# Kernel tuning notes

Hardware: AMD Instinct MI355X
Metric: run time of the kernel (lower is better)

## Reference

```python
import jax, jax.numpy as jnp
import numpy as np

HEADS = 16
HD = 64
LN_EPS = 1e-5


def swish(x):
    return x * jax.nn.sigmoid(x)


def layer_norm(x):
    mu = jnp.mean(x, axis=-1, keepdims=True)
    var = jnp.var(x, axis=-1, keepdims=True)
    return (x - mu) * jax.lax.rsqrt(var + LN_EPS)


def setup_inputs() -> dict:
    key = jax.random.key(0)
    ks = jax.random.split(key, 5)
    B, L, D = 4, 2048, 1024
    x = jax.random.normal(ks[0], (B, L, D), dtype=jnp.float32)
    W_fc = jax.random.normal(ks[1], (D, HEADS * HD * 3), dtype=jnp.float32) * (1.0 / np.sqrt(D))
    b_fc = jax.random.normal(ks[2], (HEADS * HD * 3,), dtype=jnp.float32) * 0.01
    W_fc2 = jax.random.normal(ks[3], (HEADS * HD, D), dtype=jnp.float32) * (1.0 / np.sqrt(HEADS * HD))
    b_fc2 = jax.random.normal(ks[4], (D,), dtype=jnp.float32) * 0.01
    return {"x": x, "W_fc": W_fc, "b_fc": b_fc, "W_fc2": W_fc2, "b_fc2": b_fc2}


def reference(x, W_fc, b_fc, W_fc2, b_fc2):
    B, L, D = x.shape
    # fused QKV projection with swish activation (dropout is identity in eval)
    qkv = swish(jnp.einsum('bld,de->ble', x, W_fc) + b_fc)
    qkv = qkv.reshape(B, L, HEADS, 3 * HD)
    q, k, v = jnp.split(qkv, 3, axis=-1)  # each [B, L, H, hd]
    # NOTE: original scales by sqrt(length), not sqrt(hd)
    scores = jnp.einsum('bwhd,bmhd->bhwm', q, k) / jnp.sqrt(jnp.float32(L))
    att = jax.nn.softmax(scores, axis=-1)  # [B, H, L, L]
    new_v = jnp.einsum('bhwm,bmhd->bwhd', att, v).reshape(B, L, HEADS * HD)
    m = swish(jnp.einsum('ble,ed->bld', new_v, W_fc2) + b_fc2)
    return layer_norm(x + m)
```

## Files before the change

kernel.cpp:

```cpp
#include <hip/hip_runtime.h>
#include <cstddef>
#include <cstdint>

typedef unsigned short u16;
typedef __attribute__((ext_vector_type(8))) short short8;
typedef __attribute__((ext_vector_type(4))) float floatx4;

#define C1_SCALE 0.031882111f
#define LOG2E    1.4426950408889634f

__device__ __forceinline__ u16 f2bf(float f) {
    union { float f; unsigned int i; } v; v.f = f;
    unsigned int b = v.i;
    b += 0x7FFFu + ((b >> 16) & 1u);
    return (u16)(b >> 16);
}

__device__ __forceinline__ unsigned pk2bf(float lo, float hi) {
#if __has_builtin(__builtin_amdgcn_cvt_pk_bf16_f32)
    auto v = __builtin_amdgcn_cvt_pk_bf16_f32(lo, hi);
    union { decltype(v) b; unsigned u; } c; c.b = v; return c.u;
#else
    return (unsigned)f2bf(lo) | ((unsigned)f2bf(hi) << 16);
#endif
}
__device__ __forceinline__ int4 pack8bf(float4 a, float4 b) {
    union { unsigned u[4]; int4 v; } c;
    c.u[0] = pk2bf(a.x, a.y); c.u[1] = pk2bf(a.z, a.w);
    c.u[2] = pk2bf(b.x, b.y); c.u[3] = pk2bf(b.z, b.w);
    return c.v;
}
__device__ __forceinline__ float fastrcp(float x) {
#if __has_builtin(__builtin_amdgcn_rcpf)
    return __builtin_amdgcn_rcpf(x);
#else
    return 1.0f / x;
#endif
}
__device__ __forceinline__ float swishf(float s) {
    float e = __builtin_amdgcn_exp2f(-s * LOG2E);
    return s * fastrcp(1.0f + e);
}
__device__ __forceinline__ void glds16(const void* g, void* l) {
    __builtin_amdgcn_global_load_lds(
        (const __attribute__((address_space(1))) void*)g,
        (__attribute__((address_space(3))) void*)l, 16, 0, 0);
}

__global__ __launch_bounds__(256) void prep_kernel(
    const float* __restrict__ x,     u16* __restrict__ xb,
    const float* __restrict__ W_fc,  u16* __restrict__ WfcT,
    const float* __restrict__ W_fc2, u16* __restrict__ Wfc2T)
{
    const int id = blockIdx.x;
    if (id < 4096) {
        const size_t i = ((size_t)id * 256 + threadIdx.x) * 8;
        float4 a = *(const float4*)&x[i];
        float4 b = *(const float4*)&x[i + 4];
        *(int4*)&xb[i] = pack8bf(a, b);
        return;
    }
    __shared__ u16 t[32][33];
    const float* src; u16* dst; int R, C, bx, by;
    if (id < 7168) {
        const int w = id - 4096;
        bx = w % 96; by = w / 96; src = W_fc; dst = WfcT; R = 1024; C = 3072;
    } else {
        const int w = id - 7168;
        bx = w % 32; by = w / 32; src = W_fc2; dst = Wfc2T; R = 1024; C = 1024;
    }
    const int tx = threadIdx.x & 31, ty = threadIdx.x >> 5;
    const int r0 = by * 32, c0 = bx * 32;
#pragma unroll
    for (int i = 0; i < 4; ++i)
        t[ty + i * 8][tx] = f2bf(src[(size_t)(r0 + ty + i * 8) * C + c0 + tx]);
    __syncthreads();
#pragma unroll
    for (int i = 0; i < 4; ++i)
        dst[(size_t)(c0 + ty + i * 8) * R + r0 + tx] = t[tx][ty + i * 8];
}

#define GEMM_STAGE(AP, BP, Kdim)                                              \
    {                                                                          \
        _Pragma("unroll")                                                      \
        for (int i = 0; i < 4; ++i) {                                          \
            const int row = i * 32 + (tid >> 3);                               \
            const int gp  = (tid & 7) ^ (row & 7);                             \
            glds16(&AP[(size_t)(row0 + row) * Kdim + k0 + gp * 8],             \
                   &As[i * 32 + wid * 8][0]);                                  \
            glds16(&BP[(size_t)(col0 + row) * Kdim + k0 + gp * 8],             \
                   &Bs[i * 32 + wid * 8][0]);                                  \
        }                                                                      \
    }

#define GEMM_COMPUTE()                                                         \
    {                                                                          \
        _Pragma("unroll")                                                      \
        for (int kc = 0; kc < 2; ++kc) {                                       \
            short8 af[4], bf[4];                                               \
            const int gl = ((kc * 4 + quad) ^ (l16 & 7)) * 8;                  \
            _Pragma("unroll")                                                  \
            for (int mt = 0; mt < 4; ++mt)                                     \
                af[mt] = *(const short8*)&As[wm * 64 + mt * 16 + l16][gl];     \
            _Pragma("unroll")                                                  \
            for (int nt = 0; nt < 4; ++nt)                                     \
                bf[nt] = *(const short8*)&Bs[wn * 64 + nt * 16 + l16][gl];     \
            _Pragma("unroll")                                                  \
            for (int mt = 0; mt < 4; ++mt)                                     \
                _Pragma("unroll")                                              \
                for (int nt = 0; nt < 4; ++nt)                                 \
                    acc[mt][nt] = __builtin_amdgcn_mfma_f32_16x16x32_bf16(     \
                        af[mt], bf[nt], acc[mt][nt], 0, 0, 0);                 \
        }                                                                      \
    }

__global__ __launch_bounds__(256) void gemm_qkv_kernel(
    const u16* __restrict__ A, const u16* __restrict__ BT,
    const float* __restrict__ bias, u16* __restrict__ qk, u16* __restrict__ vT)
{
    const int K = 1024;
    const int tid  = threadIdx.x;
    const int wid  = tid >> 6;
    const int lane = tid & 63;
    const int quad = lane >> 4;
    const int l16  = lane & 15;
    const int wm = wid >> 1, wn = wid & 1;
    const int row0 = blockIdx.y * 128, col0 = blockIdx.x * 128;

    __shared__ __align__(16) u16 As[128][64];
    __shared__ __align__(16) u16 Bs[128][64];

    floatx4 acc[4][4] = {};

    for (int k0 = 0; k0 < K; k0 += 64) {
        if (k0) __syncthreads();
        GEMM_STAGE(A, BT, K);
        __syncthreads();
        GEMM_COMPUTE();
    }

    float bb[4];
#pragma unroll
    for (int nt = 0; nt < 4; ++nt)
        bb[nt] = bias[col0 + wn * 64 + nt * 16 + l16];

    const int b = row0 >> 11;
#pragma unroll
    for (int mt = 0; mt < 4; ++mt) {
        const int rbase = row0 + wm * 64 + mt * 16 + quad * 4;
        const int l0 = rbase & 2047;
#pragma unroll
        for (int nt = 0; nt < 4; ++nt) {
            const int c = col0 + wn * 64 + nt * 16 + l16;
            const unsigned h = (unsigned)c / 192u;
            const int w = c - (int)h * 192;
            float sw[4];
#pragma unroll
            for (int r = 0; r < 4; ++r)
                sw[r] = swishf(acc[mt][nt][r] + bb[nt]);
            if (w < 128) {
                const float scl = (w >= 64) ? C1_SCALE : 1.0f;
#pragma unroll
                for (int r = 0; r < 4; ++r)
                    qk[(size_t)(rbase + r) * 2048 + h * 128 + w] = f2bf(sw[r] * scl);
            } else {
                union { unsigned u[2]; uint2 v; } pk;
                pk.u[0] = pk2bf(sw[0], sw[1]);
                pk.u[1] = pk2bf(sw[2], sw[3]);
                *(uint2*)&vT[(size_t)((b * 16 + (int)h) * 64 + (w - 128)) * 2048 + l0] = pk.v;
            }
        }
    }
}

__global__ __launch_bounds__(256) void gemm_out_kernel(
    const u16* __restrict__ A, const u16* __restrict__ BT,
    const float* __restrict__ bias, const float* __restrict__ xres,
    float* __restrict__ out)
{
    const int K = 1024, N = 1024;
    const int tid  = threadIdx.x;
    const int wid  = tid >> 6;
    const int lane = tid & 63;
    const int quad = lane >> 4;
    const int l16  = lane & 15;
    const int wm = wid >> 1, wn = wid & 1;
    const int row0 = blockIdx.y * 128, col0 = blockIdx.x * 128;

    __shared__ __align__(16) u16 As[128][64];
    __shared__ __align__(16) u16 Bs[128][64];

    floatx4 acc[4][4] = {};

    for (int k0 = 0; k0 < K; k0 += 64) {
        if (k0) __syncthreads();
        GEMM_STAGE(A, BT, K);
        __syncthreads();
        GEMM_COMPUTE();
    }

    float bb[4];
#pragma unroll
    for (int nt = 0; nt < 4; ++nt)
        bb[nt] = bias[col0 + wn * 64 + nt * 16 + l16];

#pragma unroll
    for (int mt = 0; mt < 4; ++mt) {
#pragma unroll
        for (int nt = 0; nt < 4; ++nt) {
#pragma unroll
            for (int r = 0; r < 4; ++r) {
                int row = row0 + wm * 64 + mt * 16 + quad * 4 + r;
                int col = col0 + wn * 64 + nt * 16 + l16;
                float sw = swishf(acc[mt][nt][r] + bb[nt]);
                out[(size_t)row * N + col] = xres[(size_t)row * N + col] + sw;
            }
        }
    }
}

__global__ __launch_bounds__(256) void attn_kernel(
    const u16* __restrict__ qk, const u16* __restrict__ vT,
    u16* __restrict__ newv)
{
    const int tid  = threadIdx.x;
    const int wid  = tid >> 6;
    const int lane = tid & 63;
    const int quad = lane >> 4;
    const int l16  = lane & 15;
    const int id = blockIdx.x;
    const int qt = id >> 6;
    const int hb = id & 63;
    const int h  = hb & 15;
    const int b  = hb >> 4;

    const u16* qkb = qk + (size_t)b * 2048 * 2048;
    const u16* vTb = vT + (size_t)(b * 16 + h) * 64 * 2048;

    short8 qf[2][2];
#pragma unroll
    for (int it = 0; it < 2; ++it) {
        const int qrow = qt * 128 + (wid * 2 + it) * 16 + l16;
        const u16* qp = &qkb[(size_t)qrow * 2048 + h * 128];
        qf[it][0] = *(const short8*)&qp[quad * 8];
        qf[it][1] = *(const short8*)&qp[32 + quad * 8];
    }

    const short one = (short)0x3F80;
    const short8 ones = {one, one, one, one, one, one, one, one};

    __shared__ __align__(16) u16 Ks[128][64];
    __shared__ __align__(16) u16 Vt[64][128];
    __shared__ __align__(16) u16 Ps[4][16][64];

    const int krow_l = tid >> 3;
    const int kgp    = (tid & 7) ^ (krow_l & 7);
    const int vrow_l = tid >> 4;
    const int vg     = tid & 15;
    const int vgp    = ((vg >> 3) << 3) | ((vg & 7) ^ (vrow_l & 7));

    floatx4 oacc[2][4] = {};
    floatx4 sumacc[2] = {};

    for (int kt = 0; kt < 16; ++kt) {
        const int k0 = kt * 128;
        if (kt) __syncthreads();
#pragma unroll
        for (int c = 0; c < 4; ++c)
            glds16(&qkb[(size_t)(k0 + c * 32 + krow_l) * 2048 + h * 128 + 64 + kgp * 8],
                   &Ks[c * 32 + wid * 8][0]);
#pragma unroll
        for (int c = 0; c < 4; ++c)
            glds16(&vTb[(size_t)(c * 16 + vrow_l) * 2048 + k0 + vgp * 8],
                   &Vt[c * 16 + wid * 4][0]);
        __syncthreads();

#pragma unroll
        for (int s = 0; s < 2; ++s) {
            floatx4 sacc[2][4] = {};
#pragma unroll
            for (int kc = 0; kc < 2; ++kc) {
                const int gl = ((kc * 4 + quad) ^ (l16 & 7)) * 8;
#pragma unroll
                for (int nt = 0; nt < 4; ++nt) {
                    short8 kf = *(const short8*)&Ks[s * 64 + nt * 16 + l16][gl];
                    sacc[0][nt] = __builtin_amdgcn_mfma_f32_16x16x32_bf16(kf, qf[0][kc], sacc[0][nt], 0, 0, 0);
                    sacc[1][nt] = __builtin_amdgcn_mfma_f32_16x16x32_bf16(kf, qf[1][kc], sacc[1][nt], 0, 0, 0);
                }
            }

#pragma unroll
            for (int it = 0; it < 2; ++it) {
#pragma unroll
                for (int nt = 0; nt < 4; ++nt) {
                    float p0 = __builtin_amdgcn_exp2f(sacc[it][nt][0]);
                    float p1 = __builtin_amdgcn_exp2f(sacc[it][nt][1]);
                    float p2 = __builtin_amdgcn_exp2f(sacc[it][nt][2]);
                    float p3 = __builtin_amdgcn_exp2f(sacc[it][nt][3]);
                    union { unsigned u[2]; uint2 v; } pk;
                    pk.u[0] = pk2bf(p0, p1);
                    pk.u[1] = pk2bf(p2, p3);
                    const int col = (((nt * 2 + (quad >> 1)) ^ (l16 & 7)) * 8) + (quad & 1) * 4;
                    *(uint2*)&Ps[wid][l16][col] = pk.v;
                }
#pragma unroll
                for (int kc = 0; kc < 2; ++kc) {
                    const int gl = ((kc * 4 + quad) ^ (l16 & 7)) * 8;
                    short8 pf = *(const short8*)&Ps[wid][l16][gl];
                    sumacc[it] = __builtin_amdgcn_mfma_f32_16x16x32_bf16(ones, pf, sumacc[it], 0, 0, 0);
#pragma unroll
                    for (int nt = 0; nt < 4; ++nt) {
                        short8 vf = *(const short8*)&Vt[nt * 16 + l16][s * 64 + gl];
                        oacc[it][nt] = __builtin_amdgcn_mfma_f32_16x16x32_bf16(vf, pf, oacc[it][nt], 0, 0, 0);
                    }
                }
            }
        }
    }

#pragma unroll
    for (int it = 0; it < 2; ++it) {
        const float inv = fastrcp(sumacc[it][0]);
        const int row = qt * 128 + (wid * 2 + it) * 16 + l16;
        u16* orow = &newv[((size_t)b * 2048 + row) * 1024 + h * 64];
#pragma unroll
        for (int nt = 0; nt < 4; ++nt) {
            union { unsigned u[2]; uint2 v; } pk;
            pk.u[0] = pk2bf(oacc[it][nt][0] * inv, oacc[it][nt][1] * inv);
            pk.u[1] = pk2bf(oacc[it][nt][2] * inv, oacc[it][nt][3] * inv);
            *(uint2*)&orow[nt * 16 + quad * 4] = pk.v;
        }
    }
}

__global__ __launch_bounds__(256) void ln_kernel(
    const float* __restrict__ y, float* __restrict__ out)
{
    const int row = blockIdx.x;
    const int tid = threadIdx.x;
    const float* yr = y + (size_t)row * 1024;
    float v[4];
    float s1 = 0.f, s2 = 0.f;
#pragma unroll
    for (int i = 0; i < 4; ++i) {
        v[i] = yr[tid + i * 256];
        s1 += v[i];
        s2 += v[i] * v[i];
    }
#pragma unroll
    for (int off = 1; off < 64; off <<= 1) {
        s1 += __shfl_xor(s1, off, 64);
        s2 += __shfl_xor(s2, off, 64);
    }
    __shared__ float red1[4], red2[4];
    const int wid = tid >> 6, lane = tid & 63;
    if (lane == 0) { red1[wid] = s1; red2[wid] = s2; }
    __syncthreads();
    s1 = red1[0] + red1[1] + red1[2] + red1[3];
    s2 = red2[0] + red2[1] + red2[2] + red2[3];
    const float mu   = s1 * (1.0f / 1024.0f);
    const float var  = s2 * (1.0f / 1024.0f) - mu * mu;
    const float rstd = rsqrtf(var + 1e-5f);
    float* orow = out + (size_t)row * 1024;
#pragma unroll
    for (int i = 0; i < 4; ++i)
        orow[tid + i * 256] = (v[i] - mu) * rstd;
}

extern "C" void kernel_launch(void* const* d_in, const int* in_sizes, int n_in,
                              void* d_out, int out_size, void* d_ws, size_t ws_size,
                              hipStream_t stream) {
    const float* x     = (const float*)d_in[0];
    const float* W_fc  = (const float*)d_in[1];
    const float* b_fc  = (const float*)d_in[2];
    const float* W_fc2 = (const float*)d_in[3];
    const float* b_fc2 = (const float*)d_in[4];
    float* out = (float*)d_out;

    char* ob = (char*)d_out;
    u16* WfcT  = (u16*)ob;
    u16* Wfc2T = (u16*)(ob + 6291456);
    u16* xbf   = (u16*)(ob + 8388608);
    u16* newv  = (u16*)(ob + 8388608);

    char* ws = (char*)d_ws;
    u16*   qk = (u16*)ws;
    u16*   vT = (u16*)(ws + 33554432);
    float* y  = (float*)ws;

    prep_kernel<<<dim3(8192), 256, 0, stream>>>(x, xbf, W_fc, WfcT, W_fc2, Wfc2T);

    gemm_qkv_kernel<<<dim3(24, 64), 256, 0, stream>>>(xbf, WfcT, b_fc, qk, vT);

    attn_kernel<<<dim3(1024), 256, 0, stream>>>(qk, vT, newv);

    gemm_out_kernel<<<dim3(8, 64), 256, 0, stream>>>(newv, Wfc2T, b_fc2, x, y);

    ln_kernel<<<dim3(8192), 256, 0, stream>>>(y, out);
}
```

Before: 308.8 us.

## Stage V transpose through LDS and enlarge attention query tile per block

The QKV GEMM epilogue now writes the V portion into shared memory first, then emits coalesced 16-byte rows of the transposed V buffer instead of scattered 8-byte column writes. The attention kernel processes 256 query rows per block (64 per wave) with 64-key tiles, loads K and V fragments into registers once per tile and reuses them across four query sub-tiles, and halves the grid. This increases K/V reuse per LDS load and reduces global K/V traffic, but raises register pressure (launch bounds set to 2 blocks) and leaves fewer blocks to fill the GPU.

```diff
diff --git a/kernel.cpp b/kernel.cpp
--- a/kernel.cpp
+++ b/kernel.cpp
@@ -127,8 +127,10 @@
     const int wm = wid >> 1, wn = wid & 1;
     const int row0 = blockIdx.y * 128, col0 = blockIdx.x * 128;
 
-    __shared__ __align__(16) u16 As[128][64];
-    __shared__ __align__(16) u16 Bs[128][64];
+    __shared__ __align__(16) u16 SMEM[2][128][64];
+    auto& As = SMEM[0];
+    auto& Bs = SMEM[1];
+    u16 (*Vs)[136] = (u16(*)[136])&SMEM[0][0][0];
 
     floatx4 acc[4][4] = {};
 
@@ -144,32 +146,51 @@
     for (int nt = 0; nt < 4; ++nt)
         bb[nt] = bias[col0 + wn * 64 + nt * 16 + l16];
 
+    const int m384  = col0 % 384;
+    const bool hasv = (m384 != 0);
+    const int  vwn  = (m384 == 128) ? 0 : 1;
+    const bool kscl = (m384 == 0 && wn == 1) || (m384 == 256 && wn == 0);
+    const float scl = kscl ? C1_SCALE : 1.0f;
     const int b = row0 >> 11;
+
+    if (hasv) __syncthreads();
+
 #pragma unroll
     for (int mt = 0; mt < 4; ++mt) {
         const int rbase = row0 + wm * 64 + mt * 16 + quad * 4;
-        const int l0 = rbase & 2047;
+        const int rloc  = wm * 64 + mt * 16 + quad * 4;
 #pragma unroll
         for (int nt = 0; nt < 4; ++nt) {
-            const int c = col0 + wn * 64 + nt * 16 + l16;
-            const unsigned h = (unsigned)c / 192u;
-            const int w = c - (int)h * 192;
             float sw[4];
 #pragma unroll
             for (int r = 0; r < 4; ++r)
                 sw[r] = swishf(acc[mt][nt][r] + bb[nt]);
-            if (w < 128) {
-                const float scl = (w >= 64) ? C1_SCALE : 1.0f;
+            if (hasv && wn == vwn) {
+                union { u16 hh[4]; uint2 v; } pk;
+#pragma unroll
+                for (int r = 0; r < 4; ++r) pk.hh[r] = f2bf(sw[r]);
+                *(uint2*)&Vs[nt * 16 + l16][rloc] = pk.v;
+            } else {
+                const int c = col0 + wn * 64 + nt * 16 + l16;
+                const unsigned h = (unsigned)c / 192u;
+                const int w = c - (int)h * 192;
 #pragma unroll
                 for (int r = 0; r < 4; ++r)
                     qk[(size_t)(rbase + r) * 2048 + h * 128 + w] = f2bf(sw[r] * scl);
-            } else {
-                union { unsigned u[2]; uint2 v; } pk;
-                pk.u[0] = pk2bf(sw[0], sw[1]);
-                pk.u[1] = pk2bf(sw[2], sw[3]);
-                *(uint2*)&vT[(size_t)((b * 16 + (int)h) * 64 + (w - 128)) * 2048 + l0] = pk.v;
             }
         }
+    }
+
+    if (hasv) {
+        __syncthreads();
+        const int hv = (m384 == 128) ? (col0 / 192) : ((col0 + 64) / 192);
+        const int d  = tid >> 2;
+        const int ch = (tid & 3) * 32;
+        const int l0b = row0 & 2047;
+        u16* dst = &vT[((size_t)(b * 16 + hv) * 64 + d) * 2048 + l0b + ch];
+#pragma unroll
+        for (int q = 0; q < 4; ++q)
+            *(int4*)&dst[q * 8] = *(const int4*)&Vs[d][ch + q * 8];
     }
 }
 
@@ -219,7 +240,7 @@
     }
 }
 
-__global__ __launch_bounds__(256) void attn_kernel(
+__global__ __launch_bounds__(256, 2) void attn_kernel(
     const u16* __restrict__ qk, const u16* __restrict__ vT,
     u16* __restrict__ newv)
 {
@@ -237,10 +258,10 @@
     const u16* qkb = qk + (size_t)b * 2048 * 2048;
     const u16* vTb = vT + (size_t)(b * 16 + h) * 64 * 2048;
 
-    short8 qf[2][2];
-#pragma unroll
-    for (int it = 0; it < 2; ++it) {
-        const int qrow = qt * 128 + (wid * 2 + it) * 16 + l16;
+    short8 qf[4][2];
+#pragma unroll
+    for (int it = 0; it < 4; ++it) {
+        const int qrow = qt * 256 + wid * 64 + it * 16 + l16;
         const u16* qp = &qkb[(size_t)qrow * 2048 + h * 128];
         qf[it][0] = *(const short8*)&qp[quad * 8];
         qf[it][1] = *(const short8*)&qp[32 + quad * 8];
@@ -249,79 +270,79 @@
     const short one = (short)0x3F80;
     const short8 ones = {one, one, one, one, one, one, one, one};
 
-    __shared__ __align__(16) u16 Ks[128][64];
-    __shared__ __align__(16) u16 Vt[64][128];
+    __shared__ __align__(16) u16 Ks[64][64];
+    __shared__ __align__(16) u16 Vt[64][64];
     __shared__ __align__(16) u16 Ps[4][16][64];
 
-    const int krow_l = tid >> 3;
-    const int kgp    = (tid & 7) ^ (krow_l & 7);
-    const int vrow_l = tid >> 4;
-    const int vg     = tid & 15;
-    const int vgp    = ((vg >> 3) << 3) | ((vg & 7) ^ (vrow_l & 7));
-
-    floatx4 oacc[2][4] = {};
-    floatx4 sumacc[2] = {};
-
-    for (int kt = 0; kt < 16; ++kt) {
-        const int k0 = kt * 128;
+    const int srow = tid >> 3;
+    const int sg0  = (tid & 7) ^ (srow & 7);
+
+    floatx4 oacc[4][4] = {};
+    floatx4 sumacc[4] = {};
+
+    for (int kt = 0; kt < 32; ++kt) {
+        const int k0 = kt * 64;
         if (kt) __syncthreads();
 #pragma unroll
-        for (int c = 0; c < 4; ++c)
-            glds16(&qkb[(size_t)(k0 + c * 32 + krow_l) * 2048 + h * 128 + 64 + kgp * 8],
-                   &Ks[c * 32 + wid * 8][0]);
-#pragma unroll
-        for (int c = 0; c < 4; ++c)
-            glds16(&vTb[(size_t)(c * 16 + vrow_l) * 2048 + k0 + vgp * 8],
-                   &Vt[c * 16 + wid * 4][0]);
+        for (int i = 0; i < 2; ++i) {
+            const int row = i * 32 + srow;
+            glds16(&qkb[(size_t)(k0 + row) * 2048 + h * 128 + 64 + sg0 * 8],
+                   &Ks[i * 32 + wid * 8][0]);
+            glds16(&vTb[(size_t)row * 2048 + k0 + sg0 * 8],
+                   &Vt[i * 32 + wid * 8][0]);
+        }
         __syncthreads();
 
-#pragma unroll
-        for (int s = 0; s < 2; ++s) {
-            floatx4 sacc[2][4] = {};
+        short8 kf[2][4], vf[2][4];
+#pragma unroll
+        for (int kc = 0; kc < 2; ++kc) {
+            const int gl = ((kc * 4 + quad) ^ (l16 & 7)) * 8;
+#pragma unroll
+            for (int nt = 0; nt < 4; ++nt) {
+                kf[kc][nt] = *(const short8*)&Ks[nt * 16 + l16][gl];
+                vf[kc][nt] = *(const short8*)&Vt[nt * 16 + l16][gl];
+            }
+        }
+
+#pragma unroll
+        for (int it = 0; it < 4; ++it) {
+            floatx4 sacc[4] = {};
+#pragma unroll
+            for (int kc = 0; kc < 2; ++kc)
+#pragma unroll
+                for (int nt = 0; nt < 4; ++nt)
+                    sacc[nt] = __builtin_amdgcn_mfma_f32_16x16x32_bf16(
+                        kf[kc][nt], qf[it][kc], sacc[nt], 0, 0, 0);
+
+#pragma unroll
+            for (int nt = 0; nt < 4; ++nt) {
+                float p0 = __builtin_amdgcn_exp2f(sacc[nt][0]);
+                float p1 = __builtin_amdgcn_exp2f(sacc[nt][1]);
+                float p2 = __builtin_amdgcn_exp2f(sacc[nt][2]);
+                float p3 = __builtin_amdgcn_exp2f(sacc[nt][3]);
+                union { unsigned u[2]; uint2 v; } pk;
+                pk.u[0] = pk2bf(p0, p1);
+                pk.u[1] = pk2bf(p2, p3);
+                const int col = (((nt * 2 + (quad >> 1)) ^ (l16 & 7)) * 8) + (quad & 1) * 4;
+                *(uint2*)&Ps[wid][l16][col] = pk.v;
+            }
 #pragma unroll
             for (int kc = 0; kc < 2; ++kc) {
                 const int gl = ((kc * 4 + quad) ^ (l16 & 7)) * 8;
-#pragma unroll
-                for (int nt = 0; nt < 4; ++nt) {
-                    short8 kf = *(const short8*)&Ks[s * 64 + nt * 16 + l16][gl];
-                    sacc[0][nt] = __builtin_amdgcn_mfma_f32_16x16x32_bf16(kf, qf[0][kc], sacc[0][nt], 0, 0, 0);
-                    sacc[1][nt] = __builtin_amdgcn_mfma_f32_16x16x32_bf16(kf, qf[1][kc], sacc[1][nt], 0, 0, 0);
-                }
+                short8 pf = *(const short8*)&Ps[wid][l16][gl];
+                sumacc[it] = __builtin_amdgcn_mfma_f32_16x16x32_bf16(ones, pf, sumacc[it], 0, 0, 0);
+#pragma unroll
+                for (int nt = 0; nt < 4; ++nt)
+                    oacc[it][nt] = __builtin_amdgcn_mfma_f32_16x16x32_bf16(
+                        vf[kc][nt], pf, oacc[it][nt], 0, 0, 0);
             }
-
-#pragma unroll
-            for (int it = 0; it < 2; ++it) {
-#pragma unroll
-                for (int nt = 0; nt < 4; ++nt) {
-                    float p0 = __builtin_amdgcn_exp2f(sacc[it][nt][0]);
-                    float p1 = __builtin_amdgcn_exp2f(sacc[it][nt][1]);
-                    float p2 = __builtin_amdgcn_exp2f(sacc[it][nt][2]);
-                    float p3 = __builtin_amdgcn_exp2f(sacc[it][nt][3]);
-                    union { unsigned u[2]; uint2 v; } pk;
-                    pk.u[0] = pk2bf(p0, p1);
-                    pk.u[1] = pk2bf(p2, p3);
-                    const int col = (((nt * 2 + (quad >> 1)) ^ (l16 & 7)) * 8) + (quad & 1) * 4;
-                    *(uint2*)&Ps[wid][l16][col] = pk.v;
-                }
-#pragma unroll
-                for (int kc = 0; kc < 2; ++kc) {
-                    const int gl = ((kc * 4 + quad) ^ (l16 & 7)) * 8;
-                    short8 pf = *(const short8*)&Ps[wid][l16][gl];
-                    sumacc[it] = __builtin_amdgcn_mfma_f32_16x16x32_bf16(ones, pf, sumacc[it], 0, 0, 0);
-#pragma unroll
-                    for (int nt = 0; nt < 4; ++nt) {
-                        short8 vf = *(const short8*)&Vt[nt * 16 + l16][s * 64 + gl];
-                        oacc[it][nt] = __builtin_amdgcn_mfma_f32_16x16x32_bf16(vf, pf, oacc[it][nt], 0, 0, 0);
-                    }
-                }
-            }
-        }
-    }
-
-#pragma unroll
-    for (int it = 0; it < 2; ++it) {
+        }
+    }
+
+#pragma unroll
+    for (int it = 0; it < 4; ++it) {
         const float inv = fastrcp(sumacc[it][0]);
-        const int row = qt * 128 + (wid * 2 + it) * 16 + l16;
+        const int row = qt * 256 + wid * 64 + it * 16 + l16;
         u16* orow = &newv[((size_t)b * 2048 + row) * 1024 + h * 64];
 #pragma unroll
         for (int nt = 0; nt < 4; ++nt) {
@@ -392,7 +413,7 @@
 
     gemm_qkv_kernel<<<dim3(24, 64), 256, 0, stream>>>(xbf, WfcT, b_fc, qk, vT);
 
-    attn_kernel<<<dim3(1024), 256, 0, stream>>>(qk, vT, newv);
+    attn_kernel<<<dim3(512), 256, 0, stream>>>(qk, vT, newv);
 
     gemm_out_kernel<<<dim3(8, 64), 256, 0, stream>>>(newv, Wfc2T, b_fc2, x, y);
 
```

New measurement: 291.3 us. 5.7% less time.
